# Kernel tuning notes

Measured on AMD Instinct MI355X. Metric: run time of the kernel, lower is better.

The kernel has to match this reference:

```python
import jax, jax.numpy as jnp
import numpy as np

N_NODES = 1024
N_EDGES = 16384
BS = 16
LENIN = 8500
H = 640


def setup_inputs() -> dict:
    key = jax.random.key(0)
    ks = iter(jax.random.split(key, 32))
    def rn(shape, s=0.05):
        return jax.random.normal(next(ks), shape, jnp.float32) * s
    inp = {}
    inp["x_in"] = jax.random.normal(next(ks), (N_NODES, LENIN), jnp.float32)
    inp["edge_index"] = jax.random.randint(next(ks), (2, N_EDGES), 0, N_NODES)
    inp["gender"] = jax.random.uniform(next(ks), (BS, 1), jnp.float32)
    inp["handed"] = jax.random.uniform(next(ks), (BS, 1), jnp.float32)
    ins = [LENIN, H, H]
    for l in range(3):
        inp[f"lstm_Wih{l}"] = rn((4 * H, ins[l]))
        inp[f"lstm_Whh{l}"] = rn((4 * H, H))
        inp[f"lstm_bih{l}"] = rn((4 * H,))
        inp[f"lstm_bhh{l}"] = rn((4 * H,))
    for i, (a, b) in enumerate([(640, 320), (320, 180), (180, 90), (90, 50)], 1):
        inp[f"gcn{i}_W"] = rn((a, b))
        inp[f"gcn{i}_b"] = rn((b,))
    for i, (a, b) in enumerate([(52, 32), (32, 16), (16, 1)], 1):
        inp[f"fcn{i}_W"] = rn((b, a))
        inp[f"fcn{i}_b"] = rn((b,))
    return inp


def _lstm(x, layers):
    # unbatched torch.nn.LSTM: x is [seq, in]; gate order i,f,g,o
    for (Wih, Whh, bih, bhh) in layers:
        h_dim = Whh.shape[1]
        xW = x @ Wih.T + (bih + bhh)  # [seq, 4H], precompute input projection
        def step(carry, xw, Whh=Whh, h_dim=h_dim):
            h, c = carry
            g = xw + h @ Whh.T
            i = jax.nn.sigmoid(g[:h_dim])
            f = jax.nn.sigmoid(g[h_dim:2 * h_dim])
            gg = jnp.tanh(g[2 * h_dim:3 * h_dim])
            o = jax.nn.sigmoid(g[3 * h_dim:])
            c = f * c + i * gg
            h = o * jnp.tanh(c)
            return (h, c), h
        z = jnp.zeros((h_dim,), x.dtype)
        _, x = jax.lax.scan(step, (z, z), xW)
    return x


def _gcn(x, src, dst, W, b):
    # PyG GCNConv: self-loops already appended to src/dst; sym-normalized scatter
    n = x.shape[0]
    deg = jnp.zeros((n,), x.dtype).at[dst].add(1.0)
    dinv = jax.lax.rsqrt(deg)  # deg >= 1 via self-loops
    norm = dinv[src] * dinv[dst]
    h = x @ W
    out = jnp.zeros((n, W.shape[1]), x.dtype).at[dst].add(norm[:, None] * h[src])
    return out + b


def _bn(x):
    # F.batch_norm(training=True, no affine, no running stats): biased var, eps 1e-5
    return (x - x.mean(0)) / jnp.sqrt(x.var(0) + 1e-5)


def _forward(x_in, edge_index, gender, handed, lstm, gcns, fcns):
    n = x_in.shape[0]
    loops = jnp.arange(n, dtype=edge_index.dtype)
    src = jnp.concatenate([edge_index[0], loops])
    dst = jnp.concatenate([edge_index[1], loops])
    x = _lstm(x_in, lstm)  # [n, 640]
    for (W, b) in gcns:
        x = _bn(jax.nn.leaky_relu(_gcn(x, src, dst, W, b)))
    batch = jnp.arange(n) // (n // BS)  # contiguous graph ids, as in get_batch
    x = jax.ops.segment_sum(x, batch, num_segments=BS)  # [BS, 50]
    x = jnp.concatenate([x, gender, handed], axis=1)     # [BS, 52]
    for (W, b) in fcns:
        x = x @ W.T + b
    return x  # [BS, 1]


def reference(x_in, edge_index, gender, handed,
              lstm_Wih0, lstm_Whh0, lstm_bih0, lstm_bhh0,
              lstm_Wih1, lstm_Whh1, lstm_bih1, lstm_bhh1,
              lstm_Wih2, lstm_Whh2, lstm_bih2, lstm_bhh2,
              gcn1_W, gcn1_b, gcn2_W, gcn2_b, gcn3_W, gcn3_b, gcn4_W, gcn4_b,
              fcn1_W, fcn1_b, fcn2_W, fcn2_b, fcn3_W, fcn3_b):
    lstm = [(lstm_Wih0, lstm_Whh0, lstm_bih0, lstm_bhh0),
            (lstm_Wih1, lstm_Whh1, lstm_bih1, lstm_bhh1),
            (lstm_Wih2, lstm_Whh2, lstm_bih2, lstm_bhh2)]
    gcns = [(gcn1_W, gcn1_b), (gcn2_W, gcn2_b), (gcn3_W, gcn3_b), (gcn4_W, gcn4_b)]
    fcns = [(fcn1_W, fcn1_b), (fcn2_W, fcn2_b), (fcn3_W, fcn3_b)]
    return _forward(x_in, edge_index, gender, handed, lstm, gcns, fcns)
```

## Files before the change

kernel.cpp:

```cpp
#include <hip/hip_runtime.h>
#include <cstdint>
#include <cstddef>


typedef _Float16 f16;
typedef __attribute__((ext_vector_type(2))) _Float16 f16x2;
typedef __attribute__((ext_vector_type(8))) _Float16 f16x8;
typedef __attribute__((ext_vector_type(4))) float f32x4;

#define DEVFN static __device__ __forceinline__

DEVFN unsigned pkh2(float a, float b) {
  unsigned short lo = __builtin_bit_cast(unsigned short, (_Float16)a);
  unsigned short hi = __builtin_bit_cast(unsigned short, (_Float16)b);
  return ((unsigned)hi << 16) | (unsigned)lo;
}
DEVFN float fdot2u(unsigned a, unsigned b, float c) {
  return __builtin_amdgcn_fdot2(__builtin_bit_cast(f16x2, a),
                                __builtin_bit_cast(f16x2, b), c, false);
}
DEVFN float sigm(float x) { return 1.0f / (1.0f + __expf(-x)); }
DEVFN float tanh_(float x) {
  float a = fabsf(x);
  float e = __expf(-2.0f * a);
  float t = (1.0f - e) / (1.0f + e);
  return x < 0.0f ? -t : t;
}

DEVFN void st_llc_u32(unsigned* p, unsigned v) {
  asm volatile("global_store_dword %0, %1, off sc0 sc1"
               :: "v"(p), "v"(v) : "memory");
}
DEVFN void ld2u_llc(const unsigned* p0, const unsigned* p1,
                    unsigned& a, unsigned& b) {
  asm volatile("global_load_dword %0, %2, off sc0 sc1\n\t"
               "global_load_dword %1, %3, off sc0 sc1\n\t"
               "s_waitcnt vmcnt(0)"
               : "=&v"(a), "=&v"(b) : "v"(p0), "v"(p1) : "memory");
}
DEVFN void ld4u_llc(const unsigned* p0, const unsigned* p1,
                    const unsigned* p2, const unsigned* p3,
                    unsigned& a, unsigned& b, unsigned& c, unsigned& d) {
  asm volatile("global_load_dword %0, %4, off sc0 sc1\n\t"
               "global_load_dword %1, %5, off sc0 sc1\n\t"
               "global_load_dword %2, %6, off sc0 sc1\n\t"
               "global_load_dword %3, %7, off sc0 sc1\n\t"
               "s_waitcnt vmcnt(0)"
               : "=&v"(a), "=&v"(b), "=&v"(c), "=&v"(d)
               : "v"(p0), "v"(p1), "v"(p2), "v"(p3) : "memory");
}

__global__ void k_cvt_pad(const float* __restrict__ src, f16* __restrict__ dst,
                          int K, int KP) {
  int r = blockIdx.y;
  int k = blockIdx.x * 256 + threadIdx.x;
  if (k >= KP) return;
  float v = (k < K) ? src[(size_t)r * K + k] : 0.0f;
  dst[(size_t)r * KP + k] = (f16)v;
}

__global__ void k_vadd(const float* __restrict__ a, const float* __restrict__ b,
                       float* __restrict__ o, int n) {
  int i = blockIdx.x * 256 + threadIdx.x;
  if (i < n) o[i] = a[i] + b[i];
}

__global__ void k_zero(int* __restrict__ p, int n) {
  int i = blockIdx.x * 256 + threadIdx.x;
  if (i < n) p[i] = 0;
}

__global__ __launch_bounds__(256, 2) void k_gemm_bt_f16(
    const f16* __restrict__ A, const f16* __restrict__ B,
    const float* __restrict__ bias, float* __restrict__ C,
    int M, int N, int K) {
  __shared__ __align__(16) f16 As[128 * 32];
  __shared__ __align__(16) f16 Bs[128 * 32];
  const int tid = threadIdx.x;
  const int wave = tid >> 6, lane = tid & 63;
  const int l15 = lane & 15, l4 = lane >> 4;
  const int bm = blockIdx.y * 128, bn = blockIdx.x * 128;
  const int wm = (wave >> 1) * 64, wn = (wave & 1) * 64;
  const int srow = tid >> 2;
  const int skk = (tid & 3) * 8;
  f32x4 acc[4][4] = {};
  for (int k0 = 0; k0 < K; k0 += 32) {
    __syncthreads();
#pragma unroll
    for (int i = 0; i < 2; ++i) {
      const f16* ga = A + (size_t)(bm + i * 64 + srow) * K + (k0 + skk);
      const f16* gb = B + (size_t)(bn + i * 64 + srow) * K + (k0 + skk);
      char* la = (char*)As + i * 4096 + wave * 1024;
      char* lb = (char*)Bs + i * 4096 + wave * 1024;
      __builtin_amdgcn_global_load_lds(
          (const __attribute__((address_space(1))) void*)ga,
          (__attribute__((address_space(3))) void*)la, 16, 0, 0);
      __builtin_amdgcn_global_load_lds(
          (const __attribute__((address_space(1))) void*)gb,
          (__attribute__((address_space(3))) void*)lb, 16, 0, 0);
    }
    __syncthreads();
    f16x8 af[4], bf[4];
#pragma unroll
    for (int mi = 0; mi < 4; ++mi)
      af[mi] = *(const f16x8*)&As[(wm + mi * 16 + l15) * 32 + l4 * 8];
#pragma unroll
    for (int nj = 0; nj < 4; ++nj)
      bf[nj] = *(const f16x8*)&Bs[(wn + nj * 16 + l15) * 32 + l4 * 8];
#pragma unroll
    for (int mi = 0; mi < 4; ++mi)
#pragma unroll
      for (int nj = 0; nj < 4; ++nj)
        acc[mi][nj] = __builtin_amdgcn_mfma_f32_16x16x32_f16(
            af[mi], bf[nj], acc[mi][nj], 0, 0, 0);
  }
#pragma unroll
  for (int mi = 0; mi < 4; ++mi) {
#pragma unroll
    for (int nj = 0; nj < 4; ++nj) {
      int row = bm + wm + mi * 16 + l4 * 4;
      int col = bn + wn + nj * 16 + l15;
      float bv = bias[col];
#pragma unroll
      for (int j = 0; j < 4; ++j)
        C[(size_t)(row + j) * N + col] = acc[mi][nj][j] + bv;
    }
  }
}

#define RB 20
#define SPIN_CAP 300000
__global__ __launch_bounds__(512, 2) void k_lstm3(
    const float* __restrict__ Whh0, const float* __restrict__ Whh1,
    const float* __restrict__ Whh2,
    const f16* __restrict__ Wih1, const f16* __restrict__ Wih2,
    const float* __restrict__ xw0,
    const float* __restrict__ bsum,
    unsigned* __restrict__ tag0, unsigned* __restrict__ tag1,
    unsigned* __restrict__ tag2,
    float* __restrict__ hs2) {
  __shared__ unsigned ho2s[2][320];
  __shared__ unsigned hp2s[2][320];
  const int tid = threadIdx.x;
  const int layer = blockIdx.x / RB;
  const int role = blockIdx.x % RB;
  const int slice = tid & 15;
  const int rowg = tid >> 4;
  const int dim = role * 32 + rowg;
  const int c0 = slice * 40;

  const float* Whh = (layer == 0) ? Whh0 : (layer == 1) ? Whh1 : Whh2;
  const f16* Wih = (layer == 2) ? Wih2 : Wih1;
  unsigned* tago = (layer == 0) ? tag0 : (layer == 1) ? tag1 : tag2;
  const unsigned* tagp = (layer == 2) ? tag1 : tag0;

  unsigned wh[4][20];
#pragma unroll
  for (int g = 0; g < 4; ++g) {
    const float* wr = Whh + (size_t)(g * 640 + dim) * 640 + c0;
#pragma unroll
    for (int c = 0; c < 20; ++c) {
      float2 f = *(const float2*)(wr + 2 * c);
      wh[g][c] = pkh2(f.x, f.y);
    }
  }
  unsigned wi[4][20];
  if (layer > 0) {
#pragma unroll
    for (int g = 0; g < 4; ++g) {
      const unsigned* wr = (const unsigned*)(Wih + (size_t)(g * 640 + dim) * 640 + c0);
#pragma unroll
      for (int c = 0; c < 20; ++c) wi[g][c] = wr[c];
    }
  } else {
#pragma unroll
    for (int g = 0; g < 4; ++g)
#pragma unroll
      for (int c = 0; c < 20; ++c) wi[g][c] = 0u;
  }
  const bool isred = (slice == 0);
  float b0 = 0, b1 = 0, b2 = 0, b3 = 0;
  if (isred && layer > 0) {
    const float* br = bsum + layer * 2560 + dim;
    b0 = br[0]; b1 = br[640]; b2 = br[1280]; b3 = br[1920];
  }
  float creg = 0.0f;
  int dead = 0;
  for (int t = 0; t < 1024; ++t) {
    const int par = t & 1;
    float xwv0 = b0, xwv1 = b1, xwv2 = b2, xwv3 = b3;
    if (isred && layer == 0) {
      const float* xr = xw0 + (size_t)t * 2560 + dim;
      xwv0 = xr[0]; xwv1 = xr[640]; xwv2 = xr[1280]; xwv3 = xr[1920];
    }
    if (tid < 320) {
      const unsigned tgo = (unsigned)t;
      const unsigned tgp = (unsigned)(t + 1);
      const bool needo = (t > 0), needp = (layer > 0);
      unsigned v0 = 0, v1 = 0, v2 = 0, v3 = 0;
      if (!dead) {
        if (needo && needp) {
          const unsigned* po = tago + (size_t)(t - 1) * 640 + 2 * tid;
          const unsigned* pp = tagp + (size_t)t * 640 + 2 * tid;
          int spins = 0;
          for (;;) {
            ld4u_llc(po, po + 1, pp, pp + 1, v0, v1, v2, v3);
            if ((v0 >> 16) == tgo && (v1 >> 16) == tgo &&
                (v2 >> 16) == tgp && (v3 >> 16) == tgp) break;
            if (++spins > SPIN_CAP) { dead = 1; break; }
          }
        } else if (needo) {
          const unsigned* po = tago + (size_t)(t - 1) * 640 + 2 * tid;
          int spins = 0;
          for (;;) {
            ld2u_llc(po, po + 1, v0, v1);
            if ((v0 >> 16) == tgo && (v1 >> 16) == tgo) break;
            if (++spins > SPIN_CAP) { dead = 1; break; }
          }
        } else if (needp) {
          const unsigned* pp = tagp + (size_t)t * 640 + 2 * tid;
          int spins = 0;
          for (;;) {
            ld2u_llc(pp, pp + 1, v2, v3);
            if ((v2 >> 16) == tgp && (v3 >> 16) == tgp) break;
            if (++spins > SPIN_CAP) { dead = 1; break; }
          }
        }
      }
      ho2s[par][tid] = needo ? ((v0 & 0xffffu) | (v1 << 16)) : 0u;
      hp2s[par][tid] = (v2 & 0xffffu) | (v3 << 16);
    }
    __syncthreads();
    float a0 = 0, a1 = 0, a2 = 0, a3 = 0;
#pragma unroll
    for (int c = 0; c < 20; ++c) {
      unsigned hv = ho2s[par][slice * 20 + c];
      a0 = fdot2u(wh[0][c], hv, a0);
      a1 = fdot2u(wh[1][c], hv, a1);
      a2 = fdot2u(wh[2][c], hv, a2);
      a3 = fdot2u(wh[3][c], hv, a3);
    }
    if (layer > 0) {
#pragma unroll
      for (int c = 0; c < 20; ++c) {
        unsigned hv = hp2s[par][slice * 20 + c];
        a0 = fdot2u(wi[0][c], hv, a0);
        a1 = fdot2u(wi[1][c], hv, a1);
        a2 = fdot2u(wi[2][c], hv, a2);
        a3 = fdot2u(wi[3][c], hv, a3);
      }
    }
#pragma unroll
    for (int m = 1; m < 16; m <<= 1) {
      a0 += __shfl_xor(a0, m, 64);
      a1 += __shfl_xor(a1, m, 64);
      a2 += __shfl_xor(a2, m, 64);
      a3 += __shfl_xor(a3, m, 64);
    }
    if (isred) {
      float gi = sigm(xwv0 + a0);
      float gf = sigm(xwv1 + a1);
      float gg = tanh_(xwv2 + a2);
      float go = sigm(xwv3 + a3);
      creg = gf * creg + gi * gg;
      float h = go * tanh_(creg);
      unsigned hb = (unsigned)__builtin_bit_cast(unsigned short, (_Float16)h);
      st_llc_u32(tago + (size_t)t * 640 + dim, ((unsigned)(t + 1) << 16) | hb);
      if (layer == 2) hs2[(size_t)t * 640 + dim] = h;
    }
  }
}

#define NE 16384
#define NN 1024
#define NET (NE + NN)

__global__ void k_csr_count(const int* __restrict__ ei, int* __restrict__ cnt) {
  int i = blockIdx.x * 256 + threadIdx.x;
  if (i >= NET) return;
  int d = (i < NE) ? ei[NE + i] : (i - NE);
  atomicAdd(&cnt[d], 1);
}

__global__ __launch_bounds__(1024) void k_csr_scan(
    const int* __restrict__ cnt, int* __restrict__ offs,
    float* __restrict__ dinv) {
  __shared__ int sd[1024];
  int tid = threadIdx.x;
  int v = cnt[tid];
  dinv[tid] = rsqrtf((float)v);
  sd[tid] = v;
  __syncthreads();
  for (int o = 1; o < 1024; o <<= 1) {
    int t = (tid >= o) ? sd[tid - o] : 0;
    __syncthreads();
    sd[tid] += t;
    __syncthreads();
  }
  if (tid == 0) offs[0] = 0;
  offs[tid + 1] = sd[tid];
}

__global__ void k_csr_fill(const int* __restrict__ ei, const int* __restrict__ offs,
                           int* __restrict__ fillc, const float* __restrict__ dinv,
                           int* __restrict__ asrc, float* __restrict__ anrm) {
  int i = blockIdx.x * 256 + threadIdx.x;
  if (i >= NET) return;
  int s, d;
  if (i < NE) { s = ei[i]; d = ei[NE + i]; }
  else        { s = d = i - NE; }
  int pos = offs[d] + atomicAdd(&fillc[d], 1);
  asrc[pos] = s;
  anrm[pos] = dinv[s] * dinv[d];
}

__global__ void k_gemm_f32(const float* __restrict__ A, const float* __restrict__ W,
                           float* __restrict__ C, int M, int K, int N) {
  int n = blockIdx.x * 64 + threadIdx.x;
  int m = blockIdx.y * 4 + threadIdx.y;
  if (n >= N || m >= M) return;
  const float* ar = A + (size_t)m * K;
  float acc = 0.0f;
#pragma unroll 4
  for (int k = 0; k < K; ++k) acc = fmaf(ar[k], W[(size_t)k * N + n], acc);
  C[(size_t)m * N + n] = acc;
}

__global__ void k_gcn_agg(const float* __restrict__ h, const int* __restrict__ asrc,
                          const float* __restrict__ anrm, const int* __restrict__ offs,
                          const float* __restrict__ b, float* __restrict__ out,
                          int F) {
  int n = blockIdx.x, f = threadIdx.x;
  if (f >= F) return;
  int e0 = offs[n], e1 = offs[n + 1];
  float acc = 0.0f;
  for (int e = e0; e < e1; ++e)
    acc = fmaf(anrm[e], h[(size_t)asrc[e] * F + f], acc);
  acc += b[f];
  out[(size_t)n * F + f] = acc > 0.0f ? acc : 0.01f * acc;
}

__global__ void k_bn_stats(const float* __restrict__ x, float* __restrict__ mean,
                           float* __restrict__ rstd, int F) {
  int f = blockIdx.x, tid = threadIdx.x;
  float s = 0, s2 = 0;
  for (int n = tid; n < 1024; n += 256) {
    float v = x[(size_t)n * F + f];
    s += v;
    s2 += v * v;
  }
#pragma unroll
  for (int m = 1; m < 64; m <<= 1) {
    s += __shfl_xor(s, m, 64);
    s2 += __shfl_xor(s2, m, 64);
  }
  __shared__ float ls[4], ls2[4];
  int wv = tid >> 6;
  if ((tid & 63) == 0) { ls[wv] = s; ls2[wv] = s2; }
  __syncthreads();
  if (tid == 0) {
    float S = ls[0] + ls[1] + ls[2] + ls[3];
    float S2 = ls2[0] + ls2[1] + ls2[2] + ls2[3];
    float mu = S * (1.0f / 1024.0f);
    float var = S2 * (1.0f / 1024.0f) - mu * mu;
    mean[f] = mu;
    rstd[f] = rsqrtf(var + 1e-5f);
  }
}

__global__ void k_bn_apply(float* __restrict__ x, const float* __restrict__ mean,
                           const float* __restrict__ rstd, int F) {
  int f = blockIdx.x * 256 + threadIdx.x;
  int n = blockIdx.y;
  if (f < F) {
    size_t i = (size_t)n * F + f;
    x[i] = (x[i] - mean[f]) * rstd[f];
  }
}

__global__ __launch_bounds__(1024) void k_segfcn(
    const float* __restrict__ x,
    const float* __restrict__ gender, const float* __restrict__ handed,
    const float* __restrict__ W1, const float* __restrict__ b1,
    const float* __restrict__ W2, const float* __restrict__ b2,
    const float* __restrict__ W3, const float* __restrict__ b3,
    float* __restrict__ out) {
  __shared__ float seg[16][52];
  __shared__ float y1[16][32];
  __shared__ float y2[16][16];
  int tid = threadIdx.x;
  if (tid < 800) {
    int g = tid / 50, f = tid % 50;
    float s = 0;
    for (int i = 0; i < 64; ++i) s += x[(size_t)(g * 64 + i) * 50 + f];
    seg[g][f] = s;
  }
  if (tid < 16) { seg[tid][50] = gender[tid]; seg[tid][51] = handed[tid]; }
  __syncthreads();
  if (tid < 512) {
    int g = tid >> 5, o = tid & 31;
    float s = b1[o];
    for (int k = 0; k < 52; ++k) s += seg[g][k] * W1[o * 52 + k];
    y1[g][o] = s;
  }
  __syncthreads();
  if (tid < 256) {
    int g = tid >> 4, o = tid & 15;
    float s = b2[o];
    for (int k = 0; k < 32; ++k) s += y1[g][k] * W2[o * 32 + k];
    y2[g][o] = s;
  }
  __syncthreads();
  if (tid < 16) {
    float s = b3[0];
    for (int k = 0; k < 16; ++k) s += y2[tid][k] * W3[k];
    out[tid] = s;
  }
}

extern "C" void kernel_launch(void* const* d_in, const int* in_sizes, int n_in,
                              void* d_out, int out_size, void* d_ws, size_t ws_size,
                              hipStream_t stream) {
  const float* x_in   = (const float*)d_in[0];
  const int*   ei     = (const int*)d_in[1];
  const float* gender = (const float*)d_in[2];
  const float* handed = (const float*)d_in[3];
  const float* Wih[3] = {(const float*)d_in[4],  (const float*)d_in[8],  (const float*)d_in[12]};
  const float* Whh[3] = {(const float*)d_in[5],  (const float*)d_in[9],  (const float*)d_in[13]};
  const float* bih[3] = {(const float*)d_in[6],  (const float*)d_in[10], (const float*)d_in[14]};
  const float* bhh[3] = {(const float*)d_in[7],  (const float*)d_in[11], (const float*)d_in[15]};
  const float* gW[4]  = {(const float*)d_in[16], (const float*)d_in[18], (const float*)d_in[20], (const float*)d_in[22]};
  const float* gb[4]  = {(const float*)d_in[17], (const float*)d_in[19], (const float*)d_in[21], (const float*)d_in[23]};
  const float* fW[3]  = {(const float*)d_in[24], (const float*)d_in[26], (const float*)d_in[28]};
  const float* fb[3]  = {(const float*)d_in[25], (const float*)d_in[27], (const float*)d_in[29]};
  float* out = (float*)d_out;

  char* ws = (char*)d_ws;
  size_t off = 0;
  auto alloc = [&](size_t bytes) -> void* {
    void* p = ws + off;
    off = (off + bytes + 255) & ~(size_t)255;
    return p;
  };
  const int KP0 = 8512;
  f16*   X16   = (f16*)alloc((size_t)1024 * KP0 * 2);
  f16*   W016  = (f16*)alloc((size_t)2560 * KP0 * 2);
  f16*   W116  = (f16*)alloc((size_t)2560 * 640 * 2);
  f16*   W216  = (f16*)alloc((size_t)2560 * 640 * 2);
  float* BSUM  = (float*)alloc(3 * 2560 * 4);
  float* XW    = (float*)alloc((size_t)1024 * 2560 * 4);
  unsigned* TAGA = (unsigned*)alloc((size_t)3 * 1024 * 640 * 4);
  float* HS2   = (float*)alloc((size_t)1024 * 640 * 4);
  float* GA    = (float*)alloc((size_t)1024 * 320 * 4);
  float* GB    = (float*)alloc((size_t)1024 * 320 * 4);
  int*   CNT   = (int*)alloc(1024 * 4);
  int*   OFFS  = (int*)alloc(1025 * 4);
  int*   FILLC = (int*)alloc(1024 * 4);
  float* DINV  = (float*)alloc(1024 * 4);
  int*   ASRC  = (int*)alloc(NET * 4);
  float* ANRM  = (float*)alloc(NET * 4);
  float* MEAN  = (float*)alloc(320 * 4);
  float* RSTD  = (float*)alloc(320 * 4);
  unsigned* TAG0 = TAGA;
  unsigned* TAG1 = TAGA + (size_t)1024 * 640;
  unsigned* TAG2 = TAGA + (size_t)2 * 1024 * 640;
  (void)ws_size; (void)in_sizes; (void)n_in; (void)out_size;

  k_cvt_pad<<<dim3(34, 1024), 256, 0, stream>>>(x_in, X16, 8500, KP0);
  k_cvt_pad<<<dim3(34, 2560), 256, 0, stream>>>(Wih[0], W016, 8500, KP0);
  k_cvt_pad<<<dim3(3, 2560), 256, 0, stream>>>(Wih[1], W116, 640, 640);
  k_cvt_pad<<<dim3(3, 2560), 256, 0, stream>>>(Wih[2], W216, 640, 640);
  for (int l = 0; l < 3; ++l)
    k_vadd<<<10, 256, 0, stream>>>(bih[l], bhh[l], BSUM + l * 2560, 2560);

  k_zero<<<5, 256, 0, stream>>>(CNT, 1024);
  k_zero<<<5, 256, 0, stream>>>(FILLC, 1024);
  k_zero<<<7680, 256, 0, stream>>>((int*)TAGA, 3 * 1024 * 640);

  k_csr_count<<<68, 256, 0, stream>>>(ei, CNT);
  k_csr_scan<<<1, 1024, 0, stream>>>(CNT, OFFS, DINV);
  k_csr_fill<<<68, 256, 0, stream>>>(ei, OFFS, FILLC, DINV, ASRC, ANRM);

  k_gemm_bt_f16<<<dim3(20, 8), 256, 0, stream>>>(X16, W016, BSUM, XW, 1024, 2560, KP0);
  k_lstm3<<<60, 512, 0, stream>>>(Whh[0], Whh[1], Whh[2],
                                  W116, W216, XW, BSUM,
                                  TAG0, TAG1, TAG2, HS2);

  const float* gin = HS2;
  int Fin = 640;
  const int Fo[4] = {320, 180, 90, 50};
  for (int l = 0; l < 4; ++l) {
    int F = Fo[l];
    k_gemm_f32<<<dim3((F + 63) / 64, 256), dim3(64, 4), 0, stream>>>(gin, gW[l], GA, 1024, Fin, F);
    k_gcn_agg<<<1024, ((F + 63) / 64) * 64, 0, stream>>>(GA, ASRC, ANRM, OFFS, gb[l], GB, F);
    k_bn_stats<<<F, 256, 0, stream>>>(GB, MEAN, RSTD, F);
    k_bn_apply<<<dim3((F + 255) / 256, 1024), 256, 0, stream>>>(GB, MEAN, RSTD, F);
    gin = GB;
    Fin = F;
  }

  k_segfcn<<<1, 1024, 0, stream>>>(GB, gender, handed, fW[0], fb[0], fW[1], fb[1], fW[2], fb[2], out);
}
```

Baseline: 3.461 ms.

## Spread LSTM recurrence over more blocks and fold batchnorm into consumers

The persistent three-layer LSTM kernel now runs 40 blocks per layer, each owning 16 hidden dims with 32 lanes per row, instead of 20 blocks with 32 dims and 16 lanes. This halves per-thread register weights and per-step dot-product length, at the cost of a longer shuffle reduction and more blocks polling the inter-block tags. Separately, the batchnorm apply kernel is removed: normalization is applied on the fly while loading the next GCN GEMM's input and inside the final segment-sum, which saves four launches and a read-write pass.

```diff
diff --git a/kernel.cpp b/kernel.cpp
--- a/kernel.cpp
+++ b/kernel.cpp
@@ -128,9 +128,9 @@
   }
 }
 
-#define RB 20
+#define RPL 40
 #define SPIN_CAP 300000
-__global__ __launch_bounds__(512, 2) void k_lstm3(
+__global__ __launch_bounds__(512, 1) void k_lstm3(
     const float* __restrict__ Whh0, const float* __restrict__ Whh1,
     const float* __restrict__ Whh2,
     const f16* __restrict__ Wih1, const f16* __restrict__ Wih2,
@@ -142,41 +142,41 @@
   __shared__ unsigned ho2s[2][320];
   __shared__ unsigned hp2s[2][320];
   const int tid = threadIdx.x;
-  const int layer = blockIdx.x / RB;
-  const int role = blockIdx.x % RB;
-  const int slice = tid & 15;
-  const int rowg = tid >> 4;
-  const int dim = role * 32 + rowg;
-  const int c0 = slice * 40;
+  const int layer = blockIdx.x / RPL;
+  const int role = blockIdx.x % RPL;
+  const int slice = tid & 31;
+  const int rowg = tid >> 5;
+  const int dim = role * 16 + rowg;
+  const int c0 = slice * 20;
 
   const float* Whh = (layer == 0) ? Whh0 : (layer == 1) ? Whh1 : Whh2;
   const f16* Wih = (layer == 2) ? Wih2 : Wih1;
   unsigned* tago = (layer == 0) ? tag0 : (layer == 1) ? tag1 : tag2;
   const unsigned* tagp = (layer == 2) ? tag1 : tag0;
 
-  unsigned wh[4][20];
+  unsigned wh[4][10];
 #pragma unroll
   for (int g = 0; g < 4; ++g) {
     const float* wr = Whh + (size_t)(g * 640 + dim) * 640 + c0;
 #pragma unroll
-    for (int c = 0; c < 20; ++c) {
+    for (int c = 0; c < 10; ++c) {
       float2 f = *(const float2*)(wr + 2 * c);
       wh[g][c] = pkh2(f.x, f.y);
     }
   }
-  unsigned wi[4][20];
+  unsigned wi[4][10];
   if (layer > 0) {
 #pragma unroll
     for (int g = 0; g < 4; ++g) {
       const unsigned* wr = (const unsigned*)(Wih + (size_t)(g * 640 + dim) * 640 + c0);
 #pragma unroll
-      for (int c = 0; c < 20; ++c) wi[g][c] = wr[c];
+      for (int c = 0; c < 10; ++c) wi[g][c] = wr[c];
     }
   } else {
 #pragma unroll
     for (int g = 0; g < 4; ++g)
 #pragma unroll
-      for (int c = 0; c < 20; ++c) wi[g][c] = 0u;
+      for (int c = 0; c < 10; ++c) wi[g][c] = 0u;
   }
   const bool isred = (slice == 0);
   float b0 = 0, b1 = 0, b2 = 0, b3 = 0;
@@ -233,8 +233,8 @@
     __syncthreads();
     float a0 = 0, a1 = 0, a2 = 0, a3 = 0;
 #pragma unroll
-    for (int c = 0; c < 20; ++c) {
-      unsigned hv = ho2s[par][slice * 20 + c];
+    for (int c = 0; c < 10; ++c) {
+      unsigned hv = ho2s[par][slice * 10 + c];
       a0 = fdot2u(wh[0][c], hv, a0);
       a1 = fdot2u(wh[1][c], hv, a1);
       a2 = fdot2u(wh[2][c], hv, a2);
@@ -242,8 +242,8 @@
     }
     if (layer > 0) {
 #pragma unroll
-      for (int c = 0; c < 20; ++c) {
-        unsigned hv = hp2s[par][slice * 20 + c];
+      for (int c = 0; c < 10; ++c) {
+        unsigned hv = hp2s[par][slice * 10 + c];
         a0 = fdot2u(wi[0][c], hv, a0);
         a1 = fdot2u(wi[1][c], hv, a1);
         a2 = fdot2u(wi[2][c], hv, a2);
@@ -251,7 +251,7 @@
       }
     }
 #pragma unroll
-    for (int m = 1; m < 16; m <<= 1) {
+    for (int m = 1; m < 32; m <<= 1) {
       a0 += __shfl_xor(a0, m, 64);
       a1 += __shfl_xor(a1, m, 64);
       a2 += __shfl_xor(a2, m, 64);
@@ -315,14 +315,22 @@
 }
 
 __global__ void k_gemm_f32(const float* __restrict__ A, const float* __restrict__ W,
-                           float* __restrict__ C, int M, int K, int N) {
+                           float* __restrict__ C, int M, int K, int N,
+                           const float* __restrict__ mean,
+                           const float* __restrict__ rstd) {
   int n = blockIdx.x * 64 + threadIdx.x;
   int m = blockIdx.y * 4 + threadIdx.y;
   if (n >= N || m >= M) return;
   const float* ar = A + (size_t)m * K;
   float acc = 0.0f;
+  if (mean) {
 #pragma unroll 4
-  for (int k = 0; k < K; ++k) acc = fmaf(ar[k], W[(size_t)k * N + n], acc);
+    for (int k = 0; k < K; ++k)
+      acc = fmaf((ar[k] - mean[k]) * rstd[k], W[(size_t)k * N + n], acc);
+  } else {
+#pragma unroll 4
+    for (int k = 0; k < K; ++k) acc = fmaf(ar[k], W[(size_t)k * N + n], acc);
+  }
   C[(size_t)m * N + n] = acc;
 }
 
@@ -368,18 +376,9 @@
   }
 }
 
-__global__ void k_bn_apply(float* __restrict__ x, const float* __restrict__ mean,
-                           const float* __restrict__ rstd, int F) {
-  int f = blockIdx.x * 256 + threadIdx.x;
-  int n = blockIdx.y;
-  if (f < F) {
-    size_t i = (size_t)n * F + f;
-    x[i] = (x[i] - mean[f]) * rstd[f];
-  }
-}
-
 __global__ __launch_bounds__(1024) void k_segfcn(
     const float* __restrict__ x,
+    const float* __restrict__ mean, const float* __restrict__ rstd,
     const float* __restrict__ gender, const float* __restrict__ handed,
     const float* __restrict__ W1, const float* __restrict__ b1,
     const float* __restrict__ W2, const float* __restrict__ b2,
@@ -393,7 +392,7 @@
     int g = tid / 50, f = tid % 50;
     float s = 0;
     for (int i = 0; i < 64; ++i) s += x[(size_t)(g * 64 + i) * 50 + f];
-    seg[g][f] = s;
+    seg[g][f] = (s - 64.0f * mean[f]) * rstd[f];
   }
   if (tid < 16) { seg[tid][50] = gender[tid]; seg[tid][51] = handed[tid]; }
   __syncthreads();
@@ -482,22 +481,24 @@
   k_csr_fill<<<68, 256, 0, stream>>>(ei, OFFS, FILLC, DINV, ASRC, ANRM);
 
   k_gemm_bt_f16<<<dim3(20, 8), 256, 0, stream>>>(X16, W016, BSUM, XW, 1024, 2560, KP0);
-  k_lstm3<<<60, 512, 0, stream>>>(Whh[0], Whh[1], Whh[2],
-                                  W116, W216, XW, BSUM,
-                                  TAG0, TAG1, TAG2, HS2);
+  k_lstm3<<<3 * RPL, 512, 0, stream>>>(Whh[0], Whh[1], Whh[2],
+                                       W116, W216, XW, BSUM,
+                                       TAG0, TAG1, TAG2, HS2);
 
   const float* gin = HS2;
   int Fin = 640;
   const int Fo[4] = {320, 180, 90, 50};
   for (int l = 0; l < 4; ++l) {
     int F = Fo[l];
-    k_gemm_f32<<<dim3((F + 63) / 64, 256), dim3(64, 4), 0, stream>>>(gin, gW[l], GA, 1024, Fin, F);
+    const float* mn = (l == 0) ? nullptr : MEAN;
+    k_gemm_f32<<<dim3((F + 63) / 64, 256), dim3(64, 4), 0, stream>>>(
+        gin, gW[l], GA, 1024, Fin, F, mn, RSTD);
     k_gcn_agg<<<1024, ((F + 63) / 64) * 64, 0, stream>>>(GA, ASRC, ANRM, OFFS, gb[l], GB, F);
     k_bn_stats<<<F, 256, 0, stream>>>(GB, MEAN, RSTD, F);
-    k_bn_apply<<<dim3((F + 255) / 256, 1024), 256, 0, stream>>>(GB, MEAN, RSTD, F);
     gin = GB;
     Fin = F;
   }
 
-  k_segfcn<<<1, 1024, 0, stream>>>(GB, gender, handed, fW[0], fb[0], fW[1], fb[1], fW[2], fb[2], out);
-}
+  k_segfcn<<<1, 1024, 0, stream>>>(GB, MEAN, RSTD, gender, handed,
+                                   fW[0], fb[0], fW[1], fb[1], fW[2], fb[2], out);
+}
```

Measured after the change: 3.229 ms. 6.7% less time.
